# Kernel optimization log

Measured on AMD Instinct MI355X. Metric: run time of the kernel, lower is better.

The kernel has to match this reference:

```python
import jax, jax.numpy as jnp
import numpy as np

W_CHAMFER = (1.0, 1.0, 1.0)
W_LAPLACE = 0.5
W_MOVE = 0.1
W_EDGE = 0.1
W_NORMAL = 1.6e-4
W_CONST = 1.0
LAP_CONST = (0.2, 1.0, 1.0)
EPS = 1e-12


def _normalize(x):
    # F.normalize(x, dim=-1): x / max(||x||, eps)
    n = jnp.sqrt(jnp.sum(x * x, axis=-1, keepdims=True))
    return x / jnp.maximum(n, EPS)


def _pairwise_sq(x, y):
    # x: (B,N,3), y: (B,M,3) -> (B,N,M) squared distances, GEMM form
    x2 = jnp.sum(x * x, -1)
    y2 = jnp.sum(y * y, -1)
    xy = jnp.einsum('bnd,bmd->bnm', x, y)
    return x2[:, :, None] + y2[:, None, :] - 2.0 * xy


def _laplace_coord(pts, lap_idx):
    # pts: (B,V,3); lap_idx: (V,10) = [8 neighbor idx (-1 invalid), self, count]
    idx = lap_idx[:, :8]
    mask = idx < 0
    safe = jnp.where(mask, 0, idx)
    nbrs = pts[:, safe]                                  # (B,V,8,3)
    nbrs = jnp.where(mask[None, :, :, None], 0.0, nbrs)
    count = lap_idx[:, -1].astype(pts.dtype)
    return pts - nbrs.sum(2) / count[None, :, None]


def setup_inputs():
    key = jax.random.key(0)
    B, M = 2, 8192
    Vs = (642, 2562, 10242)
    Es = (1920, 7680, 30720)
    ks = jax.random.split(key, 3 + 4 * 3)
    inp = {}
    inp['gt_coord'] = jax.random.normal(ks[0], (B, M, 3), jnp.float32)
    inp['gt_normal'] = _normalize(jax.random.normal(ks[1], (B, M, 3), jnp.float32))
    for i, (V, E) in enumerate(zip(Vs, Es)):
        k0, k1, k2, k3 = ks[3 + 4 * i], ks[4 + 4 * i], ks[5 + 4 * i], ks[6 + 4 * i]
        inp[f'pred_coord_{i}'] = jax.random.normal(k0, (B, V, 3), jnp.float32)
        inp[f'pred_before_{i}'] = inp[f'pred_coord_{i}'] + 0.05 * jax.random.normal(k1, (B, V, 3), jnp.float32)
        inp[f'edges_{i}'] = jax.random.randint(k2, (E, 2), 0, V)
        nbr = jax.random.randint(k3, (V, 8), 0, V)
        nbr = nbr.at[:, 6:].set(-1)                      # 6 valid neighbors, 2 invalid slots
        self_idx = jnp.arange(V)[:, None]
        count = jnp.full((V, 1), 6)
        inp[f'laplace_idx_{i}'] = jnp.concatenate([nbr, self_idx, count], axis=1)
    return inp


def reference(pred_coord_0, pred_coord_1, pred_coord_2, pred_before_0, pred_before_1, pred_before_2, gt_coord, gt_normal, laplace_idx_0, laplace_idx_1, laplace_idx_2, edges_0, edges_1, edges_2):
    preds = (pred_coord_0, pred_coord_1, pred_coord_2)
    befores = (pred_before_0, pred_before_1, pred_before_2)
    laps = (laplace_idx_0, laplace_idx_1, laplace_idx_2)
    edges_all = (edges_0, edges_1, edges_2)
    chamfer_loss = 0.0
    edge_loss = 0.0
    normal_loss = 0.0
    lap_loss = 0.0
    move_loss = 0.0
    for i in range(3):
        pred, before, lap_idx, edges = preds[i], befores[i], laps[i], edges_all[i]
        # shared pairwise distance matrix for chamfer + knn (original recomputes)
        d = _pairwise_sq(pred, gt_coord)                 # (B,V,M)
        chamfer_loss = chamfer_loss + W_CHAMFER[i] * (jnp.mean(jnp.min(d, axis=1)) + jnp.mean(jnp.min(d, axis=2)))
        knn_idx = jnp.argmin(d, axis=2)                  # (B,V): nearest gt per pred pt
        e0, e1 = edges[:, 0], edges[:, 1]
        evec = _normalize(pred[:, e0] - pred[:, e1])     # (B,E,3)
        # faithful to torch: knn.idx.flatten() then index_select -> only batch-0
        # indices ever selected since edge ids < V
        sel = knn_idx.reshape(-1)[e0]
        nrm = _normalize(gt_normal[:, sel])              # (B,E,3)
        normal_loss = normal_loss + jnp.mean(jnp.abs(jnp.sum(evec * nrm, axis=2)))
        edge_loss = edge_loss + 3.0 * jnp.mean((pred[:, e0] - pred[:, e1]) ** 2)
        l1 = _laplace_coord(before, lap_idx)
        l2 = _laplace_coord(pred, lap_idx)
        lap_loss = lap_loss + LAP_CONST[i] * 3.0 * jnp.mean((l1 - l2) ** 2)
        if i > 0:
            move_loss = move_loss + LAP_CONST[i] * 3.0 * jnp.mean((before - pred) ** 2)
    loss = chamfer_loss + W_LAPLACE * lap_loss + W_MOVE * move_loss + W_EDGE * edge_loss + W_NORMAL * normal_loss
    return W_CONST * loss
```

## Files before the change

kernel.cpp:

```cpp
#include <hip/hip_runtime.h>


#define DEV __device__ __forceinline__

typedef __attribute__((ext_vector_type(8))) short bs8;
typedef __attribute__((ext_vector_type(4))) float f32x4;

#define PA_S 55296
#define PB_S 1857536
#define PA_U 54808
#define PB_U 167448

DEV float blockReduceSum256(float v) {
    #pragma unroll
    for (int o = 32; o > 0; o >>= 1) v += __shfl_down(v, o, 64);
    __shared__ float red4[4];
    int wid = threadIdx.x >> 6;
    if ((threadIdx.x & 63) == 0) red4[wid] = v;
    __syncthreads();
    return (threadIdx.x == 0) ? (red4[0] + red4[1] + red4[2] + red4[3]) : 0.0f;
}

DEV void split3(float u, unsigned short& h, unsigned short& m, unsigned short& l) {
    unsigned a = __float_as_uint(u);
    h = (unsigned short)(a >> 16);
    float r1 = u - __uint_as_float(a & 0xFFFF0000u);
    unsigned bb = __float_as_uint(r1);
    m = (unsigned short)(bb >> 16);
    float r2 = r1 - __uint_as_float(bb & 0xFFFF0000u);
    l = (unsigned short)(__float_as_uint(r2) >> 16);
}

DEV void packGT(const float* __restrict__ gp, char* dst) {
    float x = gp[0], y = gp[1], z = gp[2];
    unsigned short hx,mx,lx, hy,my,ly, hz,mz,lz, nh,nm,nl;
    split3(x,hx,mx,lx); split3(y,hy,my,ly); split3(z,hz,mz,lz);
    float n = fmaf(x,x,fmaf(y,y,z*z));
    split3(n,nh,nm,nl);
    const short ONE = (short)0x3F80;
    bs8 w0 = {(short)hx,(short)hx,(short)mx,(short)hx,(short)lx,(short)mx,(short)hy,(short)hy};
    bs8 w1 = {(short)my,(short)hy,(short)ly,(short)my,(short)hz,(short)hz,(short)mz,(short)hz};
    bs8 w2 = {(short)lz,(short)mz,(short)nh,(short)nm,(short)nl,ONE,ONE,ONE};
    bs8 w3 = {0,0,0,0,0,0,0,0};
    *(bs8*)(dst)       = w0;
    *(bs8*)(dst + 256) = w1;
    *(bs8*)(dst + 512) = w2;
    *(bs8*)(dst + 768) = w3;
}

DEV void packVERT(const float* __restrict__ pp, char* dst) {
    float x = pp[0], y = pp[1], z = pp[2];
    unsigned short hx,mx,lx, hy,my,ly, hz,mz,lz, nh,nm,nl;
    split3(-2.f*x,hx,mx,lx); split3(-2.f*y,hy,my,ly); split3(-2.f*z,hz,mz,lz);
    float n = fmaf(x,x,fmaf(y,y,z*z));
    split3(n,nh,nm,nl);
    const short ONE = (short)0x3F80;
    bs8 w0 = {(short)hx,(short)mx,(short)hx,(short)lx,(short)hx,(short)mx,(short)hy,(short)my};
    bs8 w1 = {(short)hy,(short)ly,(short)hy,(short)my,(short)hz,(short)mz,(short)hz,(short)lz};
    bs8 w2 = {(short)hz,(short)mz,ONE,ONE,ONE,(short)nh,(short)nm,(short)nl};
    bs8 w3 = {0,0,0,0,0,0,0,0};
    *(bs8*)(dst)       = w0;
    *(bs8*)(dst + 256) = w1;
    *(bs8*)(dst + 512) = w2;
    *(bs8*)(dst + 768) = w3;
}

#define CONSUME(ACC, GG, VM) do { \
    gmin[GG][0] = fminf(gmin[GG][0], (ACC)[0]); \
    gmin[GG][1] = fminf(gmin[GG][1], (ACC)[1]); \
    gmin[GG][2] = fminf(gmin[GG][2], (ACC)[2]); \
    gmin[GG][3] = fminf(gmin[GG][3], (ACC)[3]); \
    float t_ = fminf(fminf((ACC)[0], (ACC)[1]), fminf((ACC)[2], (ACC)[3])); \
    if (B0) { \
        t_ = fmaxf(t_, 0.0f); \
        t_ = __uint_as_float((__float_as_uint(t_) & embedMask) \
                             | (unsigned)(embedBase + 4 * (GG))); \
    } \
    VM = fminf(VM, t_); \
} while (0)

template<bool B0>
DEV void mfmaLoop(const char* SA, const char* SB, float* VML16,
                  float (&gmin)[8][4], int embedBase, unsigned embedMask)
{
    const int tid = threadIdx.x;
    const int w = tid >> 6, L = tid & 63, lr = L & 15;
    const int cp = tid >> 4;
    const char* abase = SA + (w * 8) * 1024 + (L >> 4) * 256 + lr * 16;
    bs8 af[8];
    #pragma unroll
    for (int g = 0; g < 8; g++) af[g] = *(const bs8*)(abase + g * 1024);
    __syncthreads();
    const f32x4 zero = {0.f, 0.f, 0.f, 0.f};
    const char* bbase = SB + (L >> 4) * 256 + lr * 16;
    bs8 bf = *(const bs8*)(bbase);
    #pragma unroll 2
    for (int vg = 0; vg < 16; vg++) {
        bs8 bfn = bf;
        if (vg < 15) bfn = *(const bs8*)(bbase + (vg + 1) * 1024);
        float vminA = 3.0e38f, vminB = 3.0e38f;
        f32x4 accA = __builtin_amdgcn_mfma_f32_16x16x32_bf16(af[0], bf, zero, 0, 0, 0);
        f32x4 accB = __builtin_amdgcn_mfma_f32_16x16x32_bf16(af[1], bf, zero, 0, 0, 0);
        #pragma unroll
        for (int gg = 0; gg < 8; gg += 2) {
            f32x4 ca = accA;
            if (gg < 6) accA = __builtin_amdgcn_mfma_f32_16x16x32_bf16(af[gg + 2], bf, zero, 0, 0, 0);
            CONSUME(ca, gg, vminA);
            f32x4 cb = accB;
            if (gg < 6) accB = __builtin_amdgcn_mfma_f32_16x16x32_bf16(af[gg + 3], bf, zero, 0, 0, 0);
            CONSUME(cb, gg + 1, vminB);
        }
        VML16[(vg * 16 + lr) * 17 + cp] = fminf(vminA, vminB);
        bf = bfn;
    }
}

template<bool STORE>
__global__ __launch_bounds__(256, 3) void kMega2(
    const float* __restrict__ p0, const float* __restrict__ p1, const float* __restrict__ p2,
    const float* __restrict__ b0p, const float* __restrict__ b1p, const float* __restrict__ b2p,
    const int* __restrict__ l0, const int* __restrict__ l1, const int* __restrict__ l2,
    const float* __restrict__ gt, char* ws)
{
    extern __shared__ char smem[];
    int bid = blockIdx.x;
    if (bid == 0 && threadIdx.x == 0) { *(float*)ws = 0.f; *(unsigned*)(ws + 4) = 0u; }
    if (bid < 128) {
        float c = 0.0f;
        int idx = bid * 256 + threadIdx.x;
        if (idx < 26892) {
            int level, V, t;
            const float *pred, *bef; const int* lap;
            if (idx < 1284)      { level = 0; V = 642;   pred = p0; bef = b0p; lap = l0; t = idx; }
            else if (idx < 6408) { level = 1; V = 2562;  pred = p1; bef = b1p; lap = l1; t = idx - 1284; }
            else                 { level = 2; V = 10242; pred = p2; bef = b2p; lap = l2; t = idx - 6408; }
            int b = t / V;
            int v = t - b * V;
            const float* P  = pred + ((size_t)b * V + v) * 3;
            const float* Bf = bef  + ((size_t)b * V + v) * 3;
            float dx = Bf[0] - P[0], dy = Bf[1] - P[1], dz = Bf[2] - P[2];
            float sx = 0.f, sy = 0.f, sz = 0.f;
            const int* Lp = lap + v * 10;
            #pragma unroll
            for (int j = 0; j < 8; j++) {
                int n = Lp[j];
                if (n >= 0) {
                    const float* Pn = pred + ((size_t)b * V + n) * 3;
                    const float* Bn = bef  + ((size_t)b * V + n) * 3;
                    sx += Bn[0] - Pn[0]; sy += Bn[1] - Pn[1]; sz += Bn[2] - Pn[2];
                }
            }
            float invc = 1.0f / (float)Lp[9];
            float lx = dx - sx * invc, ly = dy - sy * invc, lz = dz - sz * invc;
            float sl = fmaf(lx, lx, fmaf(ly, ly, lz * lz));
            float sm = fmaf(dx, dx, fmaf(dy, dy, dz * dz));
            float lapc = (level == 0) ? 0.2f : 1.0f;
            float iBV = 1.0f / (2.0f * (float)V);
            c = sl * (0.5f * lapc * iBV) + ((level > 0) ? sm * (0.1f * lapc * iBV) : 0.0f);
        }
        c = blockReduceSum256(c);
        if (threadIdx.x == 0) ((float*)(ws + 8))[bid] = c;
        return;
    }
    int cid = bid - 128;
    int gtt = cid & 15;
    int t2 = cid >> 4;
    int b = t2 >= 55 ? 1 : 0;
    int vt = t2 - 55 * b;
    int lvl, vtl, V, padOff, nt, tb;
    if (vt < 3)       { lvl = 0; vtl = vt;      V = 642;   padOff = 0;    nt = 3;  tb = 0; }
    else if (vt < 14) { lvl = 1; vtl = vt - 3;  V = 2562;  padOff = 768;  nt = 11; tb = 3; }
    else              { lvl = 2; vtl = vt - 14; V = 10242; padOff = 3584; nt = 41; tb = 14; }
    const float* predL = lvl == 0 ? p0 : (lvl == 1 ? p1 : p2);
    char* SA  = smem;
    char* SB  = smem + 32768;
    float* VML16 = (float*)smem;
    int tid = threadIdx.x;
    {
        int v = vtl * 256 + tid;
        if (v >= V) v -= V;
        packVERT(predL + ((size_t)b * V + v) * 3, SB + (tid >> 4) * 1024 + (tid & 15) * 16);
    }
    #pragma unroll
    for (int k = 0; k < 2; k++) {
        int j = tid + k * 256;
        packGT(gt + ((size_t)b * 8192 + gtt * 512 + j) * 3, SA + (j >> 4) * 1024 + (j & 15) * 16);
    }
    __syncthreads();
    float gmin[8][4];
    #pragma unroll
    for (int g = 0; g < 8; g++) {
        gmin[g][0] = 3.0e38f; gmin[g][1] = 3.0e38f; gmin[g][2] = 3.0e38f; gmin[g][3] = 3.0e38f;
    }
    int w = tid >> 6, L = tid & 63, lg = L >> 4;
    if (b == 0) {
        unsigned mask = STORE ? 0xFFFFFF80u : 0xFFFFF800u;
        int eb = w * 32 + lg + (STORE ? 0 : (gtt << 7));
        mfmaLoop<true>(SA, SB, VML16, gmin, eb, mask);
    } else {
        mfmaLoop<false>(SA, SB, VML16, gmin, 0, 0u);
    }
    __syncthreads();
    {
        float pv = VML16[tid * 17];
        #pragma unroll
        for (int j = 1; j < 16; j++) pv = fminf(pv, VML16[tid * 17 + j]);
        int vs = b * 14080 + padOff + vtl * 256 + tid;
        if (STORE) {
            ((float*)(ws + PA_S))[(size_t)vs * 16 + gtt] = pv;
        } else {
            if (vtl * 256 + tid < V)
                atomicMin((unsigned*)(ws + PA_U) + vs, __float_as_uint(fmaxf(pv, 0.0f)));
        }
    }
    __syncthreads();
    float* GML = (float*)smem;
    #pragma unroll
    for (int gg = 0; gg < 8; gg++) {
        #pragma unroll
        for (int r = 0; r < 4; r++)
            GML[(w * 128 + gg * 16 + lg * 4 + r) * 17 + (L & 15)] = gmin[gg][r];
    }
    __syncthreads();
    {
        size_t pbBase = (size_t)b * 450560 + (lvl == 0 ? 0 : (lvl == 1 ? 24576 : 114688));
        #pragma unroll
        for (int k = 0; k < 2; k++) {
            int g = tid + k * 256;
            float q = 3.0e38f;
            #pragma unroll
            for (int cc = 0; cc < 16; cc++)
                q = fminf(q, GML[g * 17 + ((cc + tid) & 15)]);
            if (STORE) {
                ((float*)(ws + PB_S))[pbBase + (size_t)(gtt * 512 + g) * nt + vtl] = q;
            } else {
                atomicMin((unsigned*)(ws + PB_U) + (((b * 3 + lvl) << 13) + gtt * 512 + g),
                          __float_as_uint(fmaxf(q, 0.0f)));
            }
        }
    }
}

template<bool STORE>
__global__ __launch_bounds__(256) void kCombine2(
    const float* __restrict__ p0, const float* __restrict__ p1, const float* __restrict__ p2,
    const float* __restrict__ gt, char* ws)
{
    int bid = blockIdx.x, tid = threadIdx.x;
    float c = 0.0f;
    if (bid == 302) {
        if (tid < 128) c = ((float*)(ws + 8))[tid];
    } else {
        int idx = bid * 256 + tid;
        if (idx < 28160) {
            int b = idx >= 14080 ? 1 : 0;
            int q = idx - b * 14080;
            int lvl, V, lvlOff, padOff; const float* predL; float inv;
            if (q < 768)       { lvl=0; V=642;   padOff=0;    lvlOff=0;    predL=p0; inv=1.f/1284.f; }
            else if (q < 3584) { lvl=1; V=2562;  padOff=768;  lvlOff=642;  predL=p1; inv=1.f/5124.f; }
            else               { lvl=2; V=10242; padOff=3584; lvlOff=3204; predL=p2; inv=1.f/20484.f; }
            int v = q - padOff;
            if (v < V) {
                float best; int bt = 0; unsigned bits;
                if (STORE) {
                    const float4* P4 = (const float4*)((const float*)(ws + PA_S) + (size_t)idx * 16);
                    float4 a0 = P4[0], a1 = P4[1], a2 = P4[2], a3 = P4[3];
                    float vals[16] = {a0.x,a0.y,a0.z,a0.w, a1.x,a1.y,a1.z,a1.w,
                                      a2.x,a2.y,a2.z,a2.w, a3.x,a3.y,a3.z,a3.w};
                    best = vals[0];
                    #pragma unroll
                    for (int t = 1; t < 16; t++)
                        if (vals[t] < best) { best = vals[t]; bt = t; }
                    bits = __float_as_uint(best);
                } else {
                    bits = ((const unsigned*)(ws + PA_U))[idx];
                    best = __uint_as_float(bits);
                    bt = (bits >> 7) & 15;
                }
                float d;
                if (b == 0) {
                    int code = bits & 0x7F;
                    int m0 = bt * 512 + code * 4;
                    const float* pp = predL + (size_t)v * 3;
                    float px = pp[0], py = pp[1], pz = pp[2];
                    float bd = 3.0e38f; int bm = m0;
                    #pragma unroll
                    for (int u2 = 0; u2 < 4; u2++) {
                        const float* gp = gt + (size_t)(m0 + u2) * 3;
                        float dx = px - gp[0], dy = py - gp[1], dz = pz - gp[2];
                        float dd = fmaf(dx, dx, fmaf(dy, dy, dz * dz));
                        if (dd < bd) { bd = dd; bm = m0 + u2; }
                    }
                    ((int*)(ws + 1024))[lvlOff + v] = bm;
                    d = bd;
                } else {
                    d = best;
                }
                c = d * inv;
            }
        } else if (idx < 77312) {
            int r = idx - 28160;
            int b = r >= 24576 ? 1 : 0;
            int rem = r - b * 24576;
            int lvl = rem >> 13, m = rem & 8191;
            float d;
            if (STORE) {
                int nt = lvl == 0 ? 3 : (lvl == 1 ? 11 : 41);
                size_t pbBase = (size_t)b * 450560 + (lvl == 0 ? 0 : (lvl == 1 ? 24576 : 114688));
                const float* P = (const float*)(ws + PB_S) + pbBase + (size_t)m * nt;
                d = P[0];
                #pragma unroll 4
                for (int k2 = 1; k2 < nt; k2++) d = fminf(d, P[k2]);
            } else {
                d = __uint_as_float(((const unsigned*)(ws + PB_U))[((b * 3 + lvl) << 13) + m]);
            }
            c = d * (1.f / 16384.f);
        }
    }
    c = blockReduceSum256(c);
    if (tid == 0) atomicAdd((float*)ws, c);
}

__global__ __launch_bounds__(256) void kEdgeOut(
    const float* __restrict__ p0, const float* __restrict__ p1, const float* __restrict__ p2,
    const int* __restrict__ e0p, const int* __restrict__ e1p, const int* __restrict__ e2p,
    const float* __restrict__ gtn, char* ws, float* __restrict__ out)
{
    const int* knn = (const int*)(ws + 1024);
    int idx = blockIdx.x * 256 + threadIdx.x;
    float c = 0.0f;
    {
        int E, V, lvlOff, t;
        const float* pred; const int* edges;
        if (idx < 3840)       { E = 1920;  V = 642;   lvlOff = 0;    pred = p0; edges = e0p; t = idx; }
        else if (idx < 19200) { E = 7680;  V = 2562;  lvlOff = 642;  pred = p1; edges = e1p; t = idx - 3840; }
        else                  { E = 30720; V = 10242; lvlOff = 3204; pred = p2; edges = e2p; t = idx - 19200; }
        int b = t / E;
        int e = t % E;
        int a0 = edges[e * 2 + 0];
        int a1 = edges[e * 2 + 1];
        const float* P = pred + (size_t)b * V * 3;
        float dx = P[a0 * 3 + 0] - P[a1 * 3 + 0];
        float dy = P[a0 * 3 + 1] - P[a1 * 3 + 1];
        float dz = P[a0 * 3 + 2] - P[a1 * 3 + 2];
        float sq = fmaf(dx, dx, fmaf(dy, dy, dz * dz));
        float inv = 1.0f / fmaxf(sqrtf(sq), 1e-12f);
        int sel = knn[lvlOff + a0];
        const float* nr = gtn + ((size_t)b * 8192 + sel) * 3;
        float nx = nr[0], ny = nr[1], nz = nr[2];
        float invn = 1.0f / fmaxf(sqrtf(fmaf(nx, nx, fmaf(ny, ny, nz * nz))), 1e-12f);
        float dotv = fmaf(dx, nx, fmaf(dy, ny, dz * nz)) * inv * invn;
        float iBE = 1.0f / (2.0f * (float)E);
        c = sq * (0.1f * iBE) + fabsf(dotv) * (0.00016f * iBE);
    }
    c = blockReduceSum256(c);
    if (threadIdx.x == 0) {
        atomicAdd((float*)ws, c);
        __threadfence();
        unsigned t = atomicAdd((unsigned*)(ws + 4), 1u);
        if (t == 314u) out[0] = atomicAdd((float*)ws, 0.0f);
    }
}

extern "C" void kernel_launch(void* const* d_in, const int* in_sizes, int n_in,
                              void* d_out, int out_size, void* d_ws, size_t ws_size,
                              hipStream_t stream) {
    const float *gt, *gtn, *pred[3], *bef[3];
    const int *edg[3], *lapx[3];
    if (in_sizes[0] == 49152) {
        gt  = (const float*)d_in[0];
        gtn = (const float*)d_in[1];
        for (int i = 0; i < 3; i++) {
            pred[i] = (const float*)d_in[2 + 4 * i];
            bef[i]  = (const float*)d_in[3 + 4 * i];
            edg[i]  = (const int*)  d_in[4 + 4 * i];
            lapx[i] = (const int*)  d_in[5 + 4 * i];
        }
    } else {
        for (int i = 0; i < 3; i++) pred[i] = (const float*)d_in[i];
        for (int i = 0; i < 3; i++) bef[i]  = (const float*)d_in[3 + i];
        gt  = (const float*)d_in[6];
        gtn = (const float*)d_in[7];
        for (int i = 0; i < 3; i++) lapx[i] = (const int*)d_in[8 + i];
        for (int i = 0; i < 3; i++) edg[i]  = (const int*)d_in[11 + i];
    }

    char* ws = (char*)d_ws;
    bool store = ws_size >= (size_t)5462016;

    if (store) {
        kMega2<true><<<1888, 256, 49152, stream>>>(pred[0], pred[1], pred[2],
                                                   bef[0], bef[1], bef[2],
                                                   lapx[0], lapx[1], lapx[2], gt, ws);
        kCombine2<true><<<303, 256, 0, stream>>>(pred[0], pred[1], pred[2], gt, ws);
    } else {
        hipMemsetAsync(ws + PA_U, 0xFF, 364056 - PA_U, stream);
        kMega2<false><<<1888, 256, 49152, stream>>>(pred[0], pred[1], pred[2],
                                                    bef[0], bef[1], bef[2],
                                                    lapx[0], lapx[1], lapx[2], gt, ws);
        kCombine2<false><<<303, 256, 0, stream>>>(pred[0], pred[1], pred[2], gt, ws);
    }
    kEdgeOut<<<315, 256, 0, stream>>>(pred[0], pred[1], pred[2],
                                      edg[0], edg[1], edg[2], gtn, ws, (float*)d_out);
}
```

Before: 125.2 us.

## Halve GT tile per chamfer block to raise occupancy and block count

Each chamfer block now covers 256 GT points instead of 512, doubling the grid to 3648 blocks and cutting shared memory to 32 KB and gmin registers by half, with launch bounds raised to 4 blocks per SIMD. The per-vertex partial-min buffer grows to 32 slots per vertex and the embedded tile code is re-encoded with 6 bits, and kCombine2 is updated to match. The shared scratch switches from padded stride 17 to a rotated (XOR-like) index with stride 16, and the GML reduction overlaps VML16 storage to drop one barrier. This trades more blocks, more VERT packing and larger partial writes and reads for better latency hiding.

Measured after the change: 138.5 us. 1.11x slower.

```diff
diff --git a/kernel.cpp b/kernel.cpp
--- a/kernel.cpp
+++ b/kernel.cpp
@@ -7,7 +7,7 @@
 typedef __attribute__((ext_vector_type(4))) float f32x4;
 
 #define PA_S 55296
-#define PB_S 1857536
+#define PB_S 3659776
 #define PA_U 54808
 #define PB_U 167448
 
@@ -81,19 +81,20 @@
 
 template<bool B0>
 DEV void mfmaLoop(const char* SA, const char* SB, float* VML16,
-                  float (&gmin)[8][4], int embedBase, unsigned embedMask)
+                  float (&gmin)[4][4], int embedBase, unsigned embedMask)
 {
     const int tid = threadIdx.x;
     const int w = tid >> 6, L = tid & 63, lr = L & 15;
     const int cp = tid >> 4;
-    const char* abase = SA + (w * 8) * 1024 + (L >> 4) * 256 + lr * 16;
-    bs8 af[8];
+    const char* abase = SA + (w * 4) * 1024 + (L >> 4) * 256 + lr * 16;
+    bs8 af[4];
     #pragma unroll
-    for (int g = 0; g < 8; g++) af[g] = *(const bs8*)(abase + g * 1024);
+    for (int g = 0; g < 4; g++) af[g] = *(const bs8*)(abase + g * 1024);
     __syncthreads();
     const f32x4 zero = {0.f, 0.f, 0.f, 0.f};
     const char* bbase = SB + (L >> 4) * 256 + lr * 16;
     bs8 bf = *(const bs8*)(bbase);
+    const int vcol = (cp + lr) & 15;
     #pragma unroll 2
     for (int vg = 0; vg < 16; vg++) {
         bs8 bfn = bf;
@@ -101,22 +102,21 @@
         float vminA = 3.0e38f, vminB = 3.0e38f;
         f32x4 accA = __builtin_amdgcn_mfma_f32_16x16x32_bf16(af[0], bf, zero, 0, 0, 0);
         f32x4 accB = __builtin_amdgcn_mfma_f32_16x16x32_bf16(af[1], bf, zero, 0, 0, 0);
-        #pragma unroll
-        for (int gg = 0; gg < 8; gg += 2) {
-            f32x4 ca = accA;
-            if (gg < 6) accA = __builtin_amdgcn_mfma_f32_16x16x32_bf16(af[gg + 2], bf, zero, 0, 0, 0);
-            CONSUME(ca, gg, vminA);
-            f32x4 cb = accB;
-            if (gg < 6) accB = __builtin_amdgcn_mfma_f32_16x16x32_bf16(af[gg + 3], bf, zero, 0, 0, 0);
-            CONSUME(cb, gg + 1, vminB);
-        }
-        VML16[(vg * 16 + lr) * 17 + cp] = fminf(vminA, vminB);
+        f32x4 ca = accA;
+        accA = __builtin_amdgcn_mfma_f32_16x16x32_bf16(af[2], bf, zero, 0, 0, 0);
+        CONSUME(ca, 0, vminA);
+        f32x4 cb = accB;
+        accB = __builtin_amdgcn_mfma_f32_16x16x32_bf16(af[3], bf, zero, 0, 0, 0);
+        CONSUME(cb, 1, vminB);
+        CONSUME(accA, 2, vminA);
+        CONSUME(accB, 3, vminB);
+        VML16[(vg * 16 + lr) * 16 + vcol] = fminf(vminA, vminB);
         bf = bfn;
     }
 }
 
 template<bool STORE>
-__global__ __launch_bounds__(256, 3) void kMega2(
+__global__ __launch_bounds__(256, 4) void kMega2(
     const float* __restrict__ p0, const float* __restrict__ p1, const float* __restrict__ p2,
     const float* __restrict__ b0p, const float* __restrict__ b1p, const float* __restrict__ b2p,
     const int* __restrict__ l0, const int* __restrict__ l1, const int* __restrict__ l2,
@@ -163,80 +163,76 @@
         return;
     }
     int cid = bid - 128;
-    int gtt = cid & 15;
-    int t2 = cid >> 4;
+    int gtt = cid & 31;
+    int t2 = cid >> 5;
     int b = t2 >= 55 ? 1 : 0;
     int vt = t2 - 55 * b;
-    int lvl, vtl, V, padOff, nt, tb;
-    if (vt < 3)       { lvl = 0; vtl = vt;      V = 642;   padOff = 0;    nt = 3;  tb = 0; }
-    else if (vt < 14) { lvl = 1; vtl = vt - 3;  V = 2562;  padOff = 768;  nt = 11; tb = 3; }
-    else              { lvl = 2; vtl = vt - 14; V = 10242; padOff = 3584; nt = 41; tb = 14; }
+    int lvl, vtl, V, padOff, nt;
+    if (vt < 3)       { lvl = 0; vtl = vt;      V = 642;   padOff = 0;    nt = 3;  }
+    else if (vt < 14) { lvl = 1; vtl = vt - 3;  V = 2562;  padOff = 768;  nt = 11; }
+    else              { lvl = 2; vtl = vt - 14; V = 10242; padOff = 3584; nt = 41; }
     const float* predL = lvl == 0 ? p0 : (lvl == 1 ? p1 : p2);
     char* SA  = smem;
-    char* SB  = smem + 32768;
+    char* SB  = smem + 16384;
     float* VML16 = (float*)smem;
+    float* GML   = (float*)(smem + 16384);
     int tid = threadIdx.x;
     {
         int v = vtl * 256 + tid;
         if (v >= V) v -= V;
         packVERT(predL + ((size_t)b * V + v) * 3, SB + (tid >> 4) * 1024 + (tid & 15) * 16);
     }
+    {
+        packGT(gt + ((size_t)b * 8192 + gtt * 256 + tid) * 3,
+               SA + (tid >> 4) * 1024 + (tid & 15) * 16);
+    }
+    __syncthreads();
+    float gmin[4][4];
     #pragma unroll
-    for (int k = 0; k < 2; k++) {
-        int j = tid + k * 256;
-        packGT(gt + ((size_t)b * 8192 + gtt * 512 + j) * 3, SA + (j >> 4) * 1024 + (j & 15) * 16);
-    }
-    __syncthreads();
-    float gmin[8][4];
-    #pragma unroll
-    for (int g = 0; g < 8; g++) {
+    for (int g = 0; g < 4; g++) {
         gmin[g][0] = 3.0e38f; gmin[g][1] = 3.0e38f; gmin[g][2] = 3.0e38f; gmin[g][3] = 3.0e38f;
     }
     int w = tid >> 6, L = tid & 63, lg = L >> 4;
     if (b == 0) {
-        unsigned mask = STORE ? 0xFFFFFF80u : 0xFFFFF800u;
-        int eb = w * 32 + lg + (STORE ? 0 : (gtt << 7));
+        unsigned mask = STORE ? 0xFFFFFFC0u : 0xFFFFF800u;
+        int eb = w * 16 + lg + (STORE ? 0 : (gtt << 6));
         mfmaLoop<true>(SA, SB, VML16, gmin, eb, mask);
     } else {
         mfmaLoop<false>(SA, SB, VML16, gmin, 0, 0u);
     }
     __syncthreads();
     {
-        float pv = VML16[tid * 17];
+        float pv = VML16[tid * 16];
         #pragma unroll
-        for (int j = 1; j < 16; j++) pv = fminf(pv, VML16[tid * 17 + j]);
+        for (int j = 1; j < 16; j++) pv = fminf(pv, VML16[tid * 16 + j]);
         int vs = b * 14080 + padOff + vtl * 256 + tid;
         if (STORE) {
-            ((float*)(ws + PA_S))[(size_t)vs * 16 + gtt] = pv;
+            ((float*)(ws + PA_S))[(size_t)vs * 32 + gtt] = pv;
         } else {
             if (vtl * 256 + tid < V)
                 atomicMin((unsigned*)(ws + PA_U) + vs, __float_as_uint(fmaxf(pv, 0.0f)));
         }
-    }
-    __syncthreads();
-    float* GML = (float*)smem;
-    #pragma unroll
-    for (int gg = 0; gg < 8; gg++) {
         #pragma unroll
-        for (int r = 0; r < 4; r++)
-            GML[(w * 128 + gg * 16 + lg * 4 + r) * 17 + (L & 15)] = gmin[gg][r];
+        for (int gg = 0; gg < 4; gg++) {
+            #pragma unroll
+            for (int r = 0; r < 4; r++) {
+                int row = w * 64 + gg * 16 + lg * 4 + r;
+                GML[row * 16 + (((L & 15) + row) & 15)] = gmin[gg][r];
+            }
+        }
     }
     __syncthreads();
     {
+        float q = GML[tid * 16 + (tid & 15)];
+        #pragma unroll
+        for (int cc = 1; cc < 16; cc++)
+            q = fminf(q, GML[tid * 16 + ((cc + tid) & 15)]);
         size_t pbBase = (size_t)b * 450560 + (lvl == 0 ? 0 : (lvl == 1 ? 24576 : 114688));
-        #pragma unroll
-        for (int k = 0; k < 2; k++) {
-            int g = tid + k * 256;
-            float q = 3.0e38f;
-            #pragma unroll
-            for (int cc = 0; cc < 16; cc++)
-                q = fminf(q, GML[g * 17 + ((cc + tid) & 15)]);
-            if (STORE) {
-                ((float*)(ws + PB_S))[pbBase + (size_t)(gtt * 512 + g) * nt + vtl] = q;
-            } else {
-                atomicMin((unsigned*)(ws + PB_U) + (((b * 3 + lvl) << 13) + gtt * 512 + g),
-                          __float_as_uint(fmaxf(q, 0.0f)));
-            }
+        if (STORE) {
+            ((float*)(ws + PB_S))[pbBase + (size_t)(gtt * 256 + tid) * nt + vtl] = q;
+        } else {
+            atomicMin((unsigned*)(ws + PB_U) + (((b * 3 + lvl) << 13) + gtt * 256 + tid),
+                      __float_as_uint(fmaxf(q, 0.0f)));
         }
     }
 }
@@ -263,24 +259,27 @@
             if (v < V) {
                 float best; int bt = 0; unsigned bits;
                 if (STORE) {
-                    const float4* P4 = (const float4*)((const float*)(ws + PA_S) + (size_t)idx * 16);
-                    float4 a0 = P4[0], a1 = P4[1], a2 = P4[2], a3 = P4[3];
-                    float vals[16] = {a0.x,a0.y,a0.z,a0.w, a1.x,a1.y,a1.z,a1.w,
-                                      a2.x,a2.y,a2.z,a2.w, a3.x,a3.y,a3.z,a3.w};
-                    best = vals[0];
+                    const float4* P4 = (const float4*)((const float*)(ws + PA_S) + (size_t)idx * 32);
+                    best = 3.0e38f;
                     #pragma unroll
-                    for (int t = 1; t < 16; t++)
-                        if (vals[t] < best) { best = vals[t]; bt = t; }
+                    for (int t4 = 0; t4 < 8; t4++) {
+                        float4 a = P4[t4];
+                        int base = t4 * 4;
+                        if (a.x < best) { best = a.x; bt = base; }
+                        if (a.y < best) { best = a.y; bt = base + 1; }
+                        if (a.z < best) { best = a.z; bt = base + 2; }
+                        if (a.w < best) { best = a.w; bt = base + 3; }
+                    }
                     bits = __float_as_uint(best);
                 } else {
                     bits = ((const unsigned*)(ws + PA_U))[idx];
                     best = __uint_as_float(bits);
-                    bt = (bits >> 7) & 15;
+                    bt = (bits >> 6) & 31;
                 }
                 float d;
                 if (b == 0) {
-                    int code = bits & 0x7F;
-                    int m0 = bt * 512 + code * 4;
+                    int code = bits & 0x3F;
+                    int m0 = bt * 256 + code * 4;
                     const float* pp = predL + (size_t)v * 3;
                     float px = pp[0], py = pp[1], pz = pp[2];
                     float bd = 3.0e38f; int bm = m0;
@@ -386,16 +385,16 @@
     }
 
     char* ws = (char*)d_ws;
-    bool store = ws_size >= (size_t)5462016;
+    bool store = ws_size >= (size_t)7264256;
 
     if (store) {
-        kMega2<true><<<1888, 256, 49152, stream>>>(pred[0], pred[1], pred[2],
+        kMega2<true><<<3648, 256, 32768, stream>>>(pred[0], pred[1], pred[2],
                                                    bef[0], bef[1], bef[2],
                                                    lapx[0], lapx[1], lapx[2], gt, ws);
         kCombine2<true><<<303, 256, 0, stream>>>(pred[0], pred[1], pred[2], gt, ws);
     } else {
         hipMemsetAsync(ws + PA_U, 0xFF, 364056 - PA_U, stream);
-        kMega2<false><<<1888, 256, 49152, stream>>>(pred[0], pred[1], pred[2],
+        kMega2<false><<<3648, 256, 32768, stream>>>(pred[0], pred[1], pred[2],
                                                     bef[0], bef[1], bef[2],
                                                     lapx[0], lapx[1], lapx[2], gt, ws);
         kCombine2<false><<<303, 256, 0, stream>>>(pred[0], pred[1], pred[2], gt, ws);
```

## Fuse combine and edge kernels with a spin-wait flag on kNN readiness

Applied to the files above, without the earlier changes.

Merges the chamfer combine kernel and the edge/normal kernel into one 618-block launch. The first 55 combine blocks, which write the batch-0 kNN indices, increment a ready counter. Edge blocks compute their edge vectors first, then spin until that counter reaches 55 before reading kNN results. This removes one kernel launch and its inter-kernel gap. The cost is a spin-wait whose forward progress depends on producer blocks being scheduled before or alongside consumer blocks.

Measured after the change: 153.0 us. 1.22x slower.

```diff
diff --git a/kernel.cpp b/kernel.cpp
--- a/kernel.cpp
+++ b/kernel.cpp
@@ -10,6 +10,7 @@
 #define PB_S 1857536
 #define PA_U 54808
 #define PB_U 167448
+#define KNN_RDY 544
 
 DEV float blockReduceSum256(float v) {
     #pragma unroll
@@ -124,7 +125,9 @@
 {
     extern __shared__ char smem[];
     int bid = blockIdx.x;
-    if (bid == 0 && threadIdx.x == 0) { *(float*)ws = 0.f; *(unsigned*)(ws + 4) = 0u; }
+    if (bid == 0 && threadIdx.x == 0) {
+        *(float*)ws = 0.f; *(unsigned*)(ws + 4) = 0u; *(unsigned*)(ws + KNN_RDY) = 0u;
+    }
     if (bid < 128) {
         float c = 0.0f;
         int idx = bid * 256 + threadIdx.x;
@@ -167,10 +170,10 @@
     int t2 = cid >> 4;
     int b = t2 >= 55 ? 1 : 0;
     int vt = t2 - 55 * b;
-    int lvl, vtl, V, padOff, nt, tb;
-    if (vt < 3)       { lvl = 0; vtl = vt;      V = 642;   padOff = 0;    nt = 3;  tb = 0; }
-    else if (vt < 14) { lvl = 1; vtl = vt - 3;  V = 2562;  padOff = 768;  nt = 11; tb = 3; }
-    else              { lvl = 2; vtl = vt - 14; V = 10242; padOff = 3584; nt = 41; tb = 14; }
+    int lvl, vtl, V, padOff, nt;
+    if (vt < 3)       { lvl = 0; vtl = vt;      V = 642;   padOff = 0;    nt = 3;  }
+    else if (vt < 14) { lvl = 1; vtl = vt - 3;  V = 2562;  padOff = 768;  nt = 11; }
+    else              { lvl = 2; vtl = vt - 14; V = 10242; padOff = 3584; nt = 41; }
     const float* predL = lvl == 0 ? p0 : (lvl == 1 ? p1 : p2);
     char* SA  = smem;
     char* SB  = smem + 32768;
@@ -242,94 +245,93 @@
 }
 
 template<bool STORE>
-__global__ __launch_bounds__(256) void kCombine2(
+__global__ __launch_bounds__(256) void kCombineEdge(
     const float* __restrict__ p0, const float* __restrict__ p1, const float* __restrict__ p2,
-    const float* __restrict__ gt, char* ws)
+    const int* __restrict__ e0p, const int* __restrict__ e1p, const int* __restrict__ e2p,
+    const float* __restrict__ gt, const float* __restrict__ gtn,
+    char* ws, float* __restrict__ out)
 {
     int bid = blockIdx.x, tid = threadIdx.x;
     float c = 0.0f;
-    if (bid == 302) {
-        if (tid < 128) c = ((float*)(ws + 8))[tid];
+    if (bid < 303) {
+        if (bid == 302) {
+            if (tid < 128) c = ((float*)(ws + 8))[tid];
+        } else {
+            int idx = bid * 256 + tid;
+            if (idx < 28160) {
+                int b = idx >= 14080 ? 1 : 0;
+                int q = idx - b * 14080;
+                int lvl, V, lvlOff, padOff; const float* predL; float inv;
+                if (q < 768)       { lvl=0; V=642;   padOff=0;    lvlOff=0;    predL=p0; inv=1.f/1284.f; }
+                else if (q < 3584) { lvl=1; V=2562;  padOff=768;  lvlOff=642;  predL=p1; inv=1.f/5124.f; }
+                else               { lvl=2; V=10242; padOff=3584; lvlOff=3204; predL=p2; inv=1.f/20484.f; }
+                int v = q - padOff;
+                if (v < V) {
+                    float best; int bt = 0; unsigned bits;
+                    if (STORE) {
+                        const float4* P4 = (const float4*)((const float*)(ws + PA_S) + (size_t)idx * 16);
+                        float4 a0 = P4[0], a1 = P4[1], a2 = P4[2], a3 = P4[3];
+                        float vals[16] = {a0.x,a0.y,a0.z,a0.w, a1.x,a1.y,a1.z,a1.w,
+                                          a2.x,a2.y,a2.z,a2.w, a3.x,a3.y,a3.z,a3.w};
+                        best = vals[0];
+                        #pragma unroll
+                        for (int t = 1; t < 16; t++)
+                            if (vals[t] < best) { best = vals[t]; bt = t; }
+                        bits = __float_as_uint(best);
+                    } else {
+                        bits = ((const unsigned*)(ws + PA_U))[idx];
+                        best = __uint_as_float(bits);
+                        bt = (bits >> 7) & 15;
+                    }
+                    float d;
+                    if (b == 0) {
+                        int code = bits & 0x7F;
+                        int m0 = bt * 512 + code * 4;
+                        const float* pp = predL + (size_t)v * 3;
+                        float px = pp[0], py = pp[1], pz = pp[2];
+                        float bd = 3.0e38f; int bm = m0;
+                        #pragma unroll
+                        for (int u2 = 0; u2 < 4; u2++) {
+                            const float* gp = gt + (size_t)(m0 + u2) * 3;
+                            float dx = px - gp[0], dy = py - gp[1], dz = pz - gp[2];
+                            float dd = fmaf(dx, dx, fmaf(dy, dy, dz * dz));
+                            if (dd < bd) { bd = dd; bm = m0 + u2; }
+                        }
+                        ((int*)(ws + 1024))[lvlOff + v] = bm;
+                        d = bd;
+                    } else {
+                        d = best;
+                    }
+                    c = d * inv;
+                }
+            } else if (idx < 77312) {
+                int r = idx - 28160;
+                int b = r >= 24576 ? 1 : 0;
+                int rem = r - b * 24576;
+                int lvl = rem >> 13, m = rem & 8191;
+                float d;
+                if (STORE) {
+                    int nt = lvl == 0 ? 3 : (lvl == 1 ? 11 : 41);
+                    size_t pbBase = (size_t)b * 450560 + (lvl == 0 ? 0 : (lvl == 1 ? 24576 : 114688));
+                    const float* P = (const float*)(ws + PB_S) + pbBase + (size_t)m * nt;
+                    d = P[0];
+                    #pragma unroll 4
+                    for (int k2 = 1; k2 < nt; k2++) d = fminf(d, P[k2]);
+                } else {
+                    d = __uint_as_float(((const unsigned*)(ws + PB_U))[((b * 3 + lvl) << 13) + m]);
+                }
+                c = d * (1.f / 16384.f);
+            }
+        }
+        if (bid < 55) {
+            __syncthreads();
+            if (tid == 0) {
+                __threadfence();
+                atomicAdd((unsigned*)(ws + KNN_RDY), 1u);
+            }
+        }
     } else {
-        int idx = bid * 256 + tid;
-        if (idx < 28160) {
-            int b = idx >= 14080 ? 1 : 0;
-            int q = idx - b * 14080;
-            int lvl, V, lvlOff, padOff; const float* predL; float inv;
-            if (q < 768)       { lvl=0; V=642;   padOff=0;    lvlOff=0;    predL=p0; inv=1.f/1284.f; }
-            else if (q < 3584) { lvl=1; V=2562;  padOff=768;  lvlOff=642;  predL=p1; inv=1.f/5124.f; }
-            else               { lvl=2; V=10242; padOff=3584; lvlOff=3204; predL=p2; inv=1.f/20484.f; }
-            int v = q - padOff;
-            if (v < V) {
-                float best; int bt = 0; unsigned bits;
-                if (STORE) {
-                    const float4* P4 = (const float4*)((const float*)(ws + PA_S) + (size_t)idx * 16);
-                    float4 a0 = P4[0], a1 = P4[1], a2 = P4[2], a3 = P4[3];
-                    float vals[16] = {a0.x,a0.y,a0.z,a0.w, a1.x,a1.y,a1.z,a1.w,
-                                      a2.x,a2.y,a2.z,a2.w, a3.x,a3.y,a3.z,a3.w};
-                    best = vals[0];
-                    #pragma unroll
-                    for (int t = 1; t < 16; t++)
-                        if (vals[t] < best) { best = vals[t]; bt = t; }
-                    bits = __float_as_uint(best);
-                } else {
-                    bits = ((const unsigned*)(ws + PA_U))[idx];
-                    best = __uint_as_float(bits);
-                    bt = (bits >> 7) & 15;
-                }
-                float d;
-                if (b == 0) {
-                    int code = bits & 0x7F;
-                    int m0 = bt * 512 + code * 4;
-                    const float* pp = predL + (size_t)v * 3;
-                    float px = pp[0], py = pp[1], pz = pp[2];
-                    float bd = 3.0e38f; int bm = m0;
-                    #pragma unroll
-                    for (int u2 = 0; u2 < 4; u2++) {
-                        const float* gp = gt + (size_t)(m0 + u2) * 3;
-                        float dx = px - gp[0], dy = py - gp[1], dz = pz - gp[2];
-                        float dd = fmaf(dx, dx, fmaf(dy, dy, dz * dz));
-                        if (dd < bd) { bd = dd; bm = m0 + u2; }
-                    }
-                    ((int*)(ws + 1024))[lvlOff + v] = bm;
-                    d = bd;
-                } else {
-                    d = best;
-                }
-                c = d * inv;
-            }
-        } else if (idx < 77312) {
-            int r = idx - 28160;
-            int b = r >= 24576 ? 1 : 0;
-            int rem = r - b * 24576;
-            int lvl = rem >> 13, m = rem & 8191;
-            float d;
-            if (STORE) {
-                int nt = lvl == 0 ? 3 : (lvl == 1 ? 11 : 41);
-                size_t pbBase = (size_t)b * 450560 + (lvl == 0 ? 0 : (lvl == 1 ? 24576 : 114688));
-                const float* P = (const float*)(ws + PB_S) + pbBase + (size_t)m * nt;
-                d = P[0];
-                #pragma unroll 4
-                for (int k2 = 1; k2 < nt; k2++) d = fminf(d, P[k2]);
-            } else {
-                d = __uint_as_float(((const unsigned*)(ws + PB_U))[((b * 3 + lvl) << 13) + m]);
-            }
-            c = d * (1.f / 16384.f);
-        }
-    }
-    c = blockReduceSum256(c);
-    if (tid == 0) atomicAdd((float*)ws, c);
-}
-
-__global__ __launch_bounds__(256) void kEdgeOut(
-    const float* __restrict__ p0, const float* __restrict__ p1, const float* __restrict__ p2,
-    const int* __restrict__ e0p, const int* __restrict__ e1p, const int* __restrict__ e2p,
-    const float* __restrict__ gtn, char* ws, float* __restrict__ out)
-{
-    const int* knn = (const int*)(ws + 1024);
-    int idx = blockIdx.x * 256 + threadIdx.x;
-    float c = 0.0f;
-    {
+        int idx = (bid - 303) * 256 + tid;
         int E, V, lvlOff, t;
         const float* pred; const int* edges;
         if (idx < 3840)       { E = 1920;  V = 642;   lvlOff = 0;    pred = p0; edges = e0p; t = idx; }
@@ -345,6 +347,12 @@
         float dz = P[a0 * 3 + 2] - P[a1 * 3 + 2];
         float sq = fmaf(dx, dx, fmaf(dy, dy, dz * dz));
         float inv = 1.0f / fmaxf(sqrtf(sq), 1e-12f);
+        if (tid == 0) {
+            while (atomicAdd((unsigned*)(ws + KNN_RDY), 0u) < 55u) {}
+        }
+        __syncthreads();
+        __threadfence();
+        const int* knn = (const int*)(ws + 1024);
         int sel = knn[lvlOff + a0];
         const float* nr = gtn + ((size_t)b * 8192 + sel) * 3;
         float nx = nr[0], ny = nr[1], nz = nr[2];
@@ -354,11 +362,11 @@
         c = sq * (0.1f * iBE) + fabsf(dotv) * (0.00016f * iBE);
     }
     c = blockReduceSum256(c);
-    if (threadIdx.x == 0) {
+    if (tid == 0) {
         atomicAdd((float*)ws, c);
         __threadfence();
         unsigned t = atomicAdd((unsigned*)(ws + 4), 1u);
-        if (t == 314u) out[0] = atomicAdd((float*)ws, 0.0f);
+        if (t == 617u) out[0] = atomicAdd((float*)ws, 0.0f);
     }
 }
 
@@ -392,14 +400,16 @@
         kMega2<true><<<1888, 256, 49152, stream>>>(pred[0], pred[1], pred[2],
                                                    bef[0], bef[1], bef[2],
                                                    lapx[0], lapx[1], lapx[2], gt, ws);
-        kCombine2<true><<<303, 256, 0, stream>>>(pred[0], pred[1], pred[2], gt, ws);
+        kCombineEdge<true><<<618, 256, 0, stream>>>(pred[0], pred[1], pred[2],
+                                                    edg[0], edg[1], edg[2],
+                                                    gt, gtn, ws, (float*)d_out);
     } else {
         hipMemsetAsync(ws + PA_U, 0xFF, 364056 - PA_U, stream);
         kMega2<false><<<1888, 256, 49152, stream>>>(pred[0], pred[1], pred[2],
                                                     bef[0], bef[1], bef[2],
                                                     lapx[0], lapx[1], lapx[2], gt, ws);
-        kCombine2<false><<<303, 256, 0, stream>>>(pred[0], pred[1], pred[2], gt, ws);
-    }
-    kEdgeOut<<<315, 256, 0, stream>>>(pred[0], pred[1], pred[2],
-                                      edg[0], edg[1], edg[2], gtn, ws, (float*)d_out);
-}
+        kCombineEdge<false><<<618, 256, 0, stream>>>(pred[0], pred[1], pred[2],
+                                                     edg[0], edg[1], edg[2],
+                                                     gt, gtn, ws, (float*)d_out);
+    }
+}
```
